# Kernel tuning notes

Measured on AMD Instinct MI355X. Metric: run time of the kernel, lower is better.

## Reference

```python
import jax, jax.numpy as jnp
import numpy as np

B, T, NMELS = 2, 2048, 64
D, H, DH, M, L = 256, 4, 64, 384, 4
FF2 = 2 * 4 * D  # GLU doubles the 4*dim hidden


def _layernorm(x, g, b):
    m = x.mean(-1, keepdims=True)
    v = ((x - m) ** 2).mean(-1, keepdims=True)
    return (x - m) * jax.lax.rsqrt(v + 1e-5) * g + b


def _conv(h, w, groups=1, pad='VALID'):
    return jax.lax.conv_general_dilated(h, w, (1, 1), pad, feature_group_count=groups,
                                        dimension_numbers=('NCHW', 'OIHW', 'NCHW'))


def _bn(h, g, b, m, v):
    return (h - m[:, None, None]) * jax.lax.rsqrt(v[:, None, None] + 1e-5) * g[:, None, None] + b[:, None, None]


def setup_inputs():
    key = jax.random.key(0)
    ks = jax.random.split(key, 40)
    def n(i, shape, s):
        return (jax.random.normal(ks[i], shape) * s).astype(jnp.float32)
    z = lambda shape: jnp.zeros(shape, jnp.float32)
    o = lambda shape: jnp.ones(shape, jnp.float32)
    return dict(
        x=n(0, (B, T, NMELS), 1.0),
        conv0_w=n(1, (4, 1, 1, 1), 0.5),
        dw1_w=n(2, (4, 1, 3, 3), 0.3), dw1_b=z(4),
        pw1_w=n(3, (D // 2, 4, 1, 1), 0.5), pw1_b=z(D // 2),
        bn1_g=o(D // 2), bn1_b=z(D // 2), bn1_m=n(4, (D // 2,), 0.05), bn1_v=o(D // 2),
        dw2_w=n(5, (D // 2, 1, 3, 3), 0.3), dw2_b=z(D // 2),
        pw2_w=n(6, (D, D // 2, 1, 1), 0.1), pw2_b=z(D),
        bn2_g=o(D), bn2_b=z(D), bn2_m=n(7, (D,), 0.05), bn2_v=o(D),
        proj_w=n(8, (D, D), 0.06), proj_b=z(D),
        ln0_g=o(D), ln0_b=z(D),
        pos_emb=n(9, (1, T, D), 0.02),
        ln1_g=o((L, D)), ln1_b=z((L, D)),
        wq=n(10, (L, D, D), 0.06), bq=z((L, D)),
        wk=n(11, (L, D, D), 0.06), bk=z((L, D)),
        wv=n(12, (L, D, D), 0.06), bv=z((L, D)),
        wo=n(13, (L, D, D), 0.06), bo=z((L, D)),
        proj_mat=n(14, (L, M, DH), 1.0),
        ln2_g=o((L, D)), ln2_b=z((L, D)),
        ffw1=n(15, (L, D, FF2), 0.06), ffb1=z((L, FF2)),
        ffw2=n(16, (L, FF2 // 2, D), 0.03), ffb2=z((L, D)),
        clf_w1=n(17, (D, D // 2), 0.06), clf_b1=z(D // 2),
        clf_ln_g=o(D // 2), clf_ln_b=z(D // 2),
        clf_w2=n(18, (D // 2, 1), 0.09), clf_b2=z(1),
    )


def reference(x, conv0_w, dw1_w, dw1_b, pw1_w, pw1_b, bn1_g, bn1_b, bn1_m, bn1_v,
              dw2_w, dw2_b, pw2_w, pw2_b, bn2_g, bn2_b, bn2_m, bn2_v,
              proj_w, proj_b, ln0_g, ln0_b, pos_emb,
              ln1_g, ln1_b, wq, bq, wk, bk, wv, bv, wo, bo, proj_mat,
              ln2_g, ln2_b, ffw1, ffb1, ffw2, ffb2,
              clf_w1, clf_b1, clf_ln_g, clf_ln_b, clf_w2, clf_b2):
    pad1 = ((1, 1), (1, 1))
    # conv frontend: [B,T,n_mels] -> [B,1,n_mels,T]
    h = x.transpose(0, 2, 1)[:, None]
    h = _conv(h, conv0_w)
    h = _conv(h, dw1_w, groups=4, pad=pad1) + dw1_b[:, None, None]
    h = _conv(h, pw1_w) + pw1_b[:, None, None]
    h = jax.nn.relu(_bn(h, bn1_g, bn1_b, bn1_m, bn1_v))
    h = _conv(h, dw2_w, groups=D // 2, pad=pad1) + dw2_b[:, None, None]
    h = _conv(h, pw2_w) + pw2_b[:, None, None]
    h = jax.nn.relu(_bn(h, bn2_g, bn2_b, bn2_m, bn2_v))
    h = h.mean(axis=2).transpose(0, 2, 1)  # [B,T,D]
    h = h @ proj_w + proj_b
    h = _layernorm(h, ln0_g, ln0_b) + pos_emb[:, :h.shape[1]]
    # reversible Performer: streams x1 (attn) / x2 (ff), combined by sum
    x1, x2 = h, h
    dn = DH ** -0.25
    for l in range(L):
        a = _layernorm(x2, ln1_g[l], ln1_b[l])
        Bsz, N, _ = a.shape
        q = (a @ wq[l] + bq[l]).reshape(Bsz, N, H, DH).transpose(0, 2, 1, 3)
        k = (a @ wk[l] + bk[l]).reshape(Bsz, N, H, DH).transpose(0, 2, 1, 3)
        v = (a @ wv[l] + bv[l]).reshape(Bsz, N, H, DH).transpose(0, 2, 1, 3)
        # FAVOR+ generalized (ReLU) kernel feature maps, eps=1e-3
        qf = jax.nn.relu(jnp.einsum('bhnd,jd->bhnj', dn * q, proj_mat[l])) + 1e-3
        kf = jax.nn.relu(jnp.einsum('bhnd,jd->bhnj', dn * k, proj_mat[l])) + 1e-3
        d_inv = 1.0 / jnp.einsum('bhnj,bhj->bhn', qf, kf.sum(axis=2))
        ctx = jnp.einsum('bhnj,bhnd->bhjd', kf, v)
        o = jnp.einsum('bhjd,bhnj,bhn->bhnd', ctx, qf, d_inv)
        o = o.transpose(0, 2, 1, 3).reshape(Bsz, N, D)
        x1 = x1 + (o @ wo[l] + bo[l])
        f = _layernorm(x1, ln2_g[l], ln2_b[l])
        u1, u2 = jnp.split(f @ ffw1[l] + ffb1[l], 2, axis=-1)
        x2 = x2 + (jax.nn.gelu(u1, approximate=False) * u2) @ ffw2[l] + ffb2[l]
    h = x1 + x2
    c = jax.nn.relu(_layernorm(h @ clf_w1 + clf_b1, clf_ln_g, clf_ln_b))
    return (c @ clf_w2 + clf_b2)[..., 0]
```

## Files before the change

### kernel.cpp

```cpp
#include <hip/hip_runtime.h>
#include <hip/hip_bf16.h>
#include <math.h>

using bf16 = __hip_bfloat16;
typedef __attribute__((ext_vector_type(8))) short short8;
typedef __attribute__((ext_vector_type(4))) float f32x4;

__device__ __forceinline__ float tof(float x) { return x; }
__device__ __forceinline__ float tof(bf16 x) { return __bfloat162float(x); }
__device__ __forceinline__ float b2f(unsigned short u) {
  union { float f; unsigned int i; } c; c.i = ((unsigned int)u) << 16; return c.f;
}
__device__ __forceinline__ unsigned short f2bu(float v) {
  bf16 h = __float2bfloat16(v);
  return *(unsigned short*)&h;
}
__device__ __forceinline__ void sto1(float* p, float v) { *p = v; }
__device__ __forceinline__ void sto1(bf16* p, float v) { *p = __float2bfloat16(v); }

__device__ __forceinline__ float gelu_exact(float x) {
  return 0.5f * x * (1.f + erff(x * 0.70710678118654752f));
}

__device__ __forceinline__ void llds16(const bf16* g, short* l) {
  __builtin_amdgcn_global_load_lds((const __attribute__((address_space(1))) void*)g,
                                   (__attribute__((address_space(3))) void*)l, 16, 0, 0);
}

__global__ __launch_bounds__(256) void pack_qkv_kernel(
    const float* __restrict__ wq, const float* __restrict__ wk,
    const float* __restrict__ wv, bf16* __restrict__ out)
{
  int idx = blockIdx.x * 256 + threadIdx.x;
  int k = idx & 255;
  int nl = idx >> 8;
  int n = nl % 768, l = nl / 768;
  const float* src = (n < 256) ? wq : (n < 512 ? wk : wv);
  out[idx] = __float2bfloat16(src[(long)l * 65536 + k * 256 + (n & 255)]);
}

__global__ __launch_bounds__(256) void pack_qkvbias_kernel(
    const float* __restrict__ bq, const float* __restrict__ bk,
    const float* __restrict__ bv, float* __restrict__ out)
{
  int i = blockIdx.x * 256 + threadIdx.x;
  if (i >= 3072) return;
  int n = i % 768, l = i / 768;
  const float* src = (n < 256) ? bq : (n < 512 ? bk : bv);
  out[i] = src[l * 256 + (n & 255)];
}

__global__ __launch_bounds__(256) void tconv_kernel(
    const float* __restrict__ in, bf16* __restrict__ out,
    int K, int N, long sin, long sout)
{
  int l = blockIdx.z;
  int idx = blockIdx.x * 256 + threadIdx.x;
  int k = idx % K, n = idx / K;
  out[l * sout + idx] = __float2bfloat16(in[l * sin + (long)k * N + n]);
}

__global__ __launch_bounds__(256) void f2b_kernel(
    const float* __restrict__ in, bf16* __restrict__ out, int n)
{
  int i = blockIdx.x * 256 + threadIdx.x;
  if (i < n) out[i] = __float2bfloat16(in[i]);
}

__global__ __launch_bounds__(256) void sumb_kernel(
    const float* __restrict__ a, const float* __restrict__ b, bf16* __restrict__ o)
{
  int i = (blockIdx.x * 256 + threadIdx.x) * 4;
  float4 x = *(const float4*)&a[i];
  float4 y = *(const float4*)&b[i];
  ushort4 p;
  p.x = f2bu(x.x + y.x); p.y = f2bu(x.y + y.y);
  p.z = f2bu(x.z + y.z); p.w = f2bu(x.w + y.w);
  *(ushort4*)((unsigned short*)o + i) = p;
}

__global__ __launch_bounds__(256) void front1_kernel(
    const float* __restrict__ x, const float* __restrict__ c0w,
    const float* __restrict__ d1w, const float* __restrict__ d1b,
    const float* __restrict__ p1w, const float* __restrict__ p1b,
    const float* __restrict__ g1, const float* __restrict__ b1,
    const float* __restrict__ m1, const float* __restrict__ v1,
    bf16* __restrict__ A1)
{
  __shared__ float sd[256];
  __shared__ float spw[512];
  __shared__ float ss[128], st[128], sb[128];
  int tid = threadIdx.x;
  int bt = blockIdx.x;
  int b = bt >> 11, t = bt & 2047;
  if (tid < 128) {
    float s = g1[tid] * rsqrtf(v1[tid] + 1e-5f);
    ss[tid] = s;
    st[tid] = b1[tid] - m1[tid] * s;
    sb[tid] = p1b[tid];
#pragma unroll
    for (int c = 0; c < 4; ++c) spw[c * 128 + tid] = p1w[tid * 4 + c];
  }
  {
    int c = tid >> 6, f = tid & 63;
    float cw = c0w[c];
    float acc = d1b[c];
#pragma unroll
    for (int kh = 0; kh < 3; ++kh) {
      int fi = f + kh - 1;
      if (fi < 0 || fi >= 64) continue;
#pragma unroll
      for (int kw = 0; kw < 3; ++kw) {
        int ti = t + kw - 1;
        if (ti < 0 || ti >= 2048) continue;
        acc += d1w[c * 9 + kh * 3 + kw] * cw * x[((long)b * 2048 + ti) * 64 + fi];
      }
    }
    sd[c * 64 + f] = acc;
  }
  __syncthreads();
  long ob = (long)bt * 8192;
  for (int it = 0; it < 32; ++it) {
    int o = it * 256 + tid;
    int f = o >> 7, ci = o & 127;
    float pre = sb[ci];
#pragma unroll
    for (int c = 0; c < 4; ++c) pre = fmaf(spw[c * 128 + ci], sd[c * 64 + f], pre);
    A1[ob + o] = __float2bfloat16(fmaxf(fmaf(ss[ci], pre, st[ci]), 0.f));
  }
}

__global__ __launch_bounds__(256) void convtail_kernel(
    const bf16* __restrict__ A1, const float* __restrict__ w,
    const float* __restrict__ wb, const bf16* __restrict__ w2b,
    const float* __restrict__ pb, const float* __restrict__ g2,
    const float* __restrict__ b2, const float* __restrict__ m2,
    const float* __restrict__ v2, bf16* __restrict__ hconvb)
{
  __shared__ short dw2s[64 * 136];
  __shared__ short Bs[64 * 136];
  __shared__ float red[16 * 64];
  __shared__ float swf[1152];
  __shared__ float sbias[128], ssc[64], ssh[64];
  int tid = threadIdx.x;
  int lane = tid & 63, wv = tid >> 6;
  int quad = lane >> 4, l15 = lane & 15;
  int rw = (wv >> 1) * 32, cw = (wv & 1) * 32;
  int bt = blockIdx.x, b = bt >> 11, t = bt & 2047;
  for (int l = tid; l < 1152; l += 256) swf[l] = w[(l & 127) * 9 + (l >> 7)];
  if (tid < 128) sbias[tid] = wb[tid];
  __syncthreads();
  const unsigned short* A1u = (const unsigned short*)A1;
  for (int pass = 0; pass < 8; ++pass) {
    int idx = pass * 256 + tid;
    int f = idx >> 5, ci4 = (idx & 31) * 4;
    float a0 = sbias[ci4], a1 = sbias[ci4 + 1], a2 = sbias[ci4 + 2], a3 = sbias[ci4 + 3];
#pragma unroll
    for (int kh = 0; kh < 3; ++kh) {
      int fi = f + kh - 1;
      if (fi < 0 || fi >= 64) continue;
#pragma unroll
      for (int kw = 0; kw < 3; ++kw) {
        int ti = t + kw - 1;
        if (ti < 0 || ti >= 2048) continue;
        ushort4 u = *(const ushort4*)&A1u[(((long)b * 2048 + ti) * 64 + fi) * 128 + ci4];
        int wi = (kh * 3 + kw) * 128 + ci4;
        a0 = fmaf(swf[wi],     b2f(u.x), a0);
        a1 = fmaf(swf[wi + 1], b2f(u.y), a1);
        a2 = fmaf(swf[wi + 2], b2f(u.z), a2);
        a3 = fmaf(swf[wi + 3], b2f(u.w), a3);
      }
    }
    ushort4 p; p.x = f2bu(a0); p.y = f2bu(a1); p.z = f2bu(a2); p.w = f2bu(a3);
    *(ushort4*)&dw2s[f * 136 + ci4] = p;
  }
  for (int ct = 0; ct < 4; ++ct) {
    int co0 = ct * 64;
    __syncthreads();
    for (int l2 = 0; l2 < 4; ++l2) {
      int idx = l2 * 256 + tid;
      int row = idx >> 4, koff = (idx & 15) * 8;
      *(short8*)&Bs[row * 136 + koff] =
          *(const short8*)&w2b[(long)(co0 + row) * 128 + koff];
    }
    if (tid < 64) {
      int co = co0 + tid;
      float s = g2[co] * rsqrtf(v2[co] + 1e-5f);
      ssc[tid] = s;
      ssh[tid] = b2[co] - m2[co] * s + s * pb[co];
    }
    __syncthreads();
    f32x4 zv = {0.f, 0.f, 0.f, 0.f};
    f32x4 acc[2][2] = {{zv, zv}, {zv, zv}};
#pragma unroll
    for (int kc = 0; kc < 4; ++kc) {
      short8 a0 = *(const short8*)&dw2s[(rw + l15) * 136 + kc * 32 + quad * 8];
      short8 a1 = *(const short8*)&dw2s[(rw + 16 + l15) * 136 + kc * 32 + quad * 8];
      short8 b0 = *(const short8*)&Bs[(cw + l15) * 136 + kc * 32 + quad * 8];
      short8 b1 = *(const short8*)&Bs[(cw + 16 + l15) * 136 + kc * 32 + quad * 8];
      acc[0][0] = __builtin_amdgcn_mfma_f32_16x16x32_bf16(a0, b0, acc[0][0], 0, 0, 0);
      acc[0][1] = __builtin_amdgcn_mfma_f32_16x16x32_bf16(a0, b1, acc[0][1], 0, 0, 0);
      acc[1][0] = __builtin_amdgcn_mfma_f32_16x16x32_bf16(a1, b0, acc[1][0], 0, 0, 0);
      acc[1][1] = __builtin_amdgcn_mfma_f32_16x16x32_bf16(a1, b1, acc[1][1], 0, 0, 0);
    }
#pragma unroll
    for (int mi = 0; mi < 2; ++mi)
#pragma unroll
      for (int nj = 0; nj < 2; ++nj) {
        int colg = cw + nj * 16 + l15;
        float s = ssc[colg], sh = ssh[colg];
        float sum = 0.f;
#pragma unroll
        for (int r = 0; r < 4; ++r) sum += fmaxf(fmaf(s, acc[mi][nj][r], sh), 0.f);
        int rowgroup = (wv >> 1) * 8 + mi * 4 + quad;
        red[rowgroup * 64 + colg] = sum;
      }
    __syncthreads();
    if (tid < 64) {
      float s = 0.f;
#pragma unroll
      for (int r = 0; r < 16; ++r) s += red[r * 64 + tid];
      hconvb[(long)bt * 256 + co0 + tid] = __float2bfloat16(s * (1.f / 64.f));
    }
  }
}

template <typename CTy, int EPI>
__global__ __launch_bounds__(256) void mgemm_kernel(
    const bf16* __restrict__ A, const bf16* __restrict__ Bt,
    const float* __restrict__ bias, const float* __restrict__ res,
    const float* __restrict__ rowsc, CTy* __restrict__ C, bf16* __restrict__ C2,
    int K, int lda, int ldbt, int ldc,
    long sAb, long sAh, long sBb, long sBh, long sCb, long sCh,
    long sRb, long sRh, int Hdiv, float alpha)
{
  __shared__ short As[4096];
  __shared__ short Bs[4096];
  int tid = threadIdx.x;
  int lane = tid & 63, w = tid >> 6;
  int quad = lane >> 4, l15 = lane & 15;
  int rw = (w >> 1) * 32, cw = (w & 1) * 32;
  int r0 = blockIdx.x * 64, n0 = blockIdx.y * 64;
  int zb = blockIdx.z / Hdiv, zh = blockIdx.z % Hdiv;
  A += zb * sAb + zh * sAh;
  Bt += zb * sBb + zh * sBh;
  C += zb * sCb + zh * sCh;
  if (res) res += zb * sCb + zh * sCh;
  const float* rsp = rowsc ? rowsc + zb * sRb + zh * sRh : nullptr;
  f32x4 zv = {0.f, 0.f, 0.f, 0.f};
  f32x4 acc[2][2] = {{zv, zv}, {zv, zv}};
  const bf16* Ag = A + (long)(r0 + (tid >> 2)) * lda + ((tid & 3) * 8);
  const bf16* Bg = Bt + (long)(n0 + (tid >> 2)) * ldbt + ((tid & 3) * 8);
  short* Asd = &As[tid * 8];
  short* Bsd = &Bs[tid * 8];
  for (int k0 = 0; k0 < K; k0 += 64) {
    if (k0) __syncthreads();
    llds16(Ag + k0, Asd);
    llds16(Ag + k0 + 32, Asd + 2048);
    llds16(Bg + k0, Bsd);
    llds16(Bg + k0 + 32, Bsd + 2048);
    __syncthreads();
#pragma unroll
    for (int c = 0; c < 2; ++c) {
      short8 a0 = *(const short8*)&As[c * 2048 + (rw + l15) * 32 + quad * 8];
      short8 a1 = *(const short8*)&As[c * 2048 + (rw + 16 + l15) * 32 + quad * 8];
      short8 b0 = *(const short8*)&Bs[c * 2048 + (cw + l15) * 32 + quad * 8];
      short8 b1 = *(const short8*)&Bs[c * 2048 + (cw + 16 + l15) * 32 + quad * 8];
      acc[0][0] = __builtin_amdgcn_mfma_f32_16x16x32_bf16(a0, b0, acc[0][0], 0, 0, 0);
      acc[0][1] = __builtin_amdgcn_mfma_f32_16x16x32_bf16(a0, b1, acc[0][1], 0, 0, 0);
      acc[1][0] = __builtin_amdgcn_mfma_f32_16x16x32_bf16(a1, b0, acc[1][0], 0, 0, 0);
      acc[1][1] = __builtin_amdgcn_mfma_f32_16x16x32_bf16(a1, b1, acc[1][1], 0, 0, 0);
    }
  }
#pragma unroll
  for (int mi = 0; mi < 2; ++mi)
#pragma unroll
    for (int nj = 0; nj < 2; ++nj) {
      int colg = n0 + cw + nj * 16 + l15;
      float bv_ = bias ? bias[colg] : 0.f;
      int rbase = r0 + rw + mi * 16 + quad * 4;
      float ov[4];
#pragma unroll
      for (int r = 0; r < 4; ++r) {
        float v = acc[mi][nj][r];
        if constexpr (EPI == 0 || EPI == 5) {
          v += bv_;
        } else if constexpr (EPI == 1) {
          v += bv_ + res[(long)(rbase + r) * ldc + colg];
        } else if constexpr (EPI == 2 || EPI == 6) {
          v = fmaxf(v * alpha, 0.f) + 1e-3f;
        } else if constexpr (EPI == 3) {
          v *= rsp[rbase + r];
        } else if constexpr (EPI == 4) {
          v = gelu_exact(v + bv_) * res[(long)(rbase + r) * ldc + colg];
        }
        ov[r] = v;
      }
      if constexpr (EPI == 6) {
        ushort4 p;
        p.x = f2bu(ov[0]); p.y = f2bu(ov[1]); p.z = f2bu(ov[2]); p.w = f2bu(ov[3]);
        *(ushort4*)((unsigned short*)C + (long)colg * ldc + rbase) = p;
      } else if constexpr (EPI == 5) {
        if (colg < 512) {
#pragma unroll
          for (int r = 0; r < 4; ++r) sto1(&C[(long)(rbase + r) * ldc + colg], ov[r]);
        } else {
          int bb = rbase >> 11, t0 = rbase & 2047;
          long off = (((long)bb * 4 + ((colg - 512) >> 6)) * 64 + (colg & 63)) * 2048 + t0;
          ushort4 p;
          p.x = f2bu(ov[0]); p.y = f2bu(ov[1]); p.z = f2bu(ov[2]); p.w = f2bu(ov[3]);
          *(ushort4*)((unsigned short*)C2 + off) = p;
        }
      } else {
#pragma unroll
        for (int r = 0; r < 4; ++r) sto1(&C[(long)(rbase + r) * ldc + colg], ov[r]);
      }
    }
  (void)alpha;
}

template <int DIM, bool RELU, bool ADDPOS, bool DUAL, typename OTy>
__global__ __launch_bounds__(256) void ln_kernel(
    const float* __restrict__ in, const float* __restrict__ g,
    const float* __restrict__ b, const float* __restrict__ pos,
    OTy* __restrict__ out0, float* __restrict__ out1)
{
  constexpr int CH = DIM / 64;
  int row = blockIdx.x * 4 + (threadIdx.x >> 6);
  int lane = threadIdx.x & 63;
  const float* rp = in + (long)row * DIM + lane * CH;
  float v[CH];
#pragma unroll
  for (int i = 0; i < CH; ++i) v[i] = rp[i];
  float s = 0.f;
#pragma unroll
  for (int i = 0; i < CH; ++i) s += v[i];
#pragma unroll
  for (int o = 32; o > 0; o >>= 1) s += __shfl_xor(s, o, 64);
  float mean = s * (1.f / DIM);
  float q = 0.f;
#pragma unroll
  for (int i = 0; i < CH; ++i) { float d = v[i] - mean; q += d * d; }
#pragma unroll
  for (int o = 32; o > 0; o >>= 1) q += __shfl_xor(q, o, 64);
  float rstd = rsqrtf(q * (1.f / DIM) + 1e-5f);
  int t = row & 2047;
#pragma unroll
  for (int i = 0; i < CH; ++i) {
    int c = lane * CH + i;
    float o = (v[i] - mean) * rstd * g[c] + b[c];
    if constexpr (ADDPOS) o += pos[(long)t * DIM + c];
    if constexpr (RELU) o = fmaxf(o, 0.f);
    sto1(&out0[(long)row * DIM + c], o);
    if constexpr (DUAL) out1[(long)row * DIM + c] = o;
  }
}

__global__ __launch_bounds__(256) void rowsum_kernel(
    const bf16* __restrict__ kfT, float* __restrict__ ksum)
{
  int z = blockIdx.x;
  int j = blockIdx.y * 4 + (threadIdx.x >> 6);
  int lane = threadIdx.x & 63;
  const short* base = (const short*)kfT + ((long)z * 384 + j) * 2048;
  float acc = 0.f;
#pragma unroll
  for (int i = 0; i < 4; ++i) {
    short8 v = *(const short8*)&base[i * 512 + lane * 8];
#pragma unroll
    for (int e = 0; e < 8; ++e) acc += b2f((unsigned short)v[e]);
  }
#pragma unroll
  for (int o = 32; o > 0; o >>= 1) acc += __shfl_xor(acc, o, 64);
  if (lane == 0) ksum[z * 384 + j] = acc;
}

__global__ __launch_bounds__(256) void dinv_kernel(
    const bf16* __restrict__ qf, const float* __restrict__ ksum,
    float* __restrict__ dinv)
{
  int z = blockIdx.x;
  int t = blockIdx.y * 4 + (threadIdx.x >> 6);
  int lane = threadIdx.x & 63;
  const bf16* qr = qf + ((long)z * 2048 + t) * 384;
  const float* ks = ksum + z * 384;
  float acc = 0.f;
#pragma unroll
  for (int i = 0; i < 6; ++i) {
    int j = lane + i * 64;
    acc = fmaf(tof(qr[j]), ks[j], acc);
  }
#pragma unroll
  for (int o = 32; o > 0; o >>= 1) acc += __shfl_xor(acc, o, 64);
  if (lane == 0) dinv[z * 2048 + t] = 1.f / acc;
}

__global__ __launch_bounds__(256) void clf2_kernel(
    const float* __restrict__ c2, const float* __restrict__ w,
    const float* __restrict__ b, float* __restrict__ out)
{
  int row = blockIdx.x * 4 + (threadIdx.x >> 6);
  int lane = threadIdx.x & 63;
  const float* rp = c2 + (long)row * 128 + lane * 2;
  float acc = rp[0] * w[lane * 2] + rp[1] * w[lane * 2 + 1];
#pragma unroll
  for (int o = 32; o > 0; o >>= 1) acc += __shfl_xor(acc, o, 64);
  if (lane == 0) out[row] = acc + b[0];
}

extern "C" void kernel_launch(void* const* d_in, const int* in_sizes, int n_in,
                              void* d_out, int out_size, void* d_ws, size_t ws_size,
                              hipStream_t stream)
{
  const float* X    = (const float*)d_in[0];
  const float* c0w  = (const float*)d_in[1];
  const float* d1w  = (const float*)d_in[2];
  const float* d1b  = (const float*)d_in[3];
  const float* p1w  = (const float*)d_in[4];
  const float* p1b  = (const float*)d_in[5];
  const float* g1   = (const float*)d_in[6];
  const float* b1   = (const float*)d_in[7];
  const float* m1   = (const float*)d_in[8];
  const float* v1   = (const float*)d_in[9];
  const float* d2w  = (const float*)d_in[10];
  const float* d2b  = (const float*)d_in[11];
  const float* p2w  = (const float*)d_in[12];
  const float* p2b  = (const float*)d_in[13];
  const float* g2   = (const float*)d_in[14];
  const float* b2   = (const float*)d_in[15];
  const float* m2   = (const float*)d_in[16];
  const float* v2   = (const float*)d_in[17];
  const float* projw= (const float*)d_in[18];
  const float* projb= (const float*)d_in[19];
  const float* ln0g = (const float*)d_in[20];
  const float* ln0b = (const float*)d_in[21];
  const float* pos  = (const float*)d_in[22];
  const float* ln1g = (const float*)d_in[23];
  const float* ln1b = (const float*)d_in[24];
  const float* wq   = (const float*)d_in[25];
  const float* bq   = (const float*)d_in[26];
  const float* wk   = (const float*)d_in[27];
  const float* bk   = (const float*)d_in[28];
  const float* wv   = (const float*)d_in[29];
  const float* bv   = (const float*)d_in[30];
  const float* wo   = (const float*)d_in[31];
  const float* bo   = (const float*)d_in[32];
  const float* pmat = (const float*)d_in[33];
  const float* ln2g = (const float*)d_in[34];
  const float* ln2b = (const float*)d_in[35];
  const float* ffw1 = (const float*)d_in[36];
  const float* ffb1 = (const float*)d_in[37];
  const float* ffw2 = (const float*)d_in[38];
  const float* ffb2 = (const float*)d_in[39];
  const float* cw1  = (const float*)d_in[40];
  const float* cb1  = (const float*)d_in[41];
  const float* clng = (const float*)d_in[42];
  const float* clnb = (const float*)d_in[43];
  const float* cw2  = (const float*)d_in[44];
  const float* cb2  = (const float*)d_in[45];
  (void)in_sizes; (void)n_in; (void)out_size; (void)ws_size;

  float* ws     = (float*)d_ws;
  float* x1     = ws;
  float* x2     = ws + 1048576;
  float* lnb32  = ws + 2097152;
  bf16*  lnb16  = (bf16*)(ws + 3145728);
  bf16*  hconvb = (bf16*)(ws + 3407872);
  bf16*  obufb  = (bf16*)(ws + 3670016);
  bf16*  qkvb   = (bf16*)(ws + 3932160);
  bf16*  vT     = (bf16*)(ws + 5505024);
  bf16*  qf     = (bf16*)(ws + 6029312);
  bf16*  kfT    = (bf16*)(ws + 9175040);
  bf16*  ctxT   = (bf16*)(ws + 12320768);
  float* ksum   = ws + 12419072;
  float* dinvp  = ws + 12423168;
  float* gbuf   = ws + 12439552;
  bf16*  gb2    = (bf16*)(ws + 16633856);
  bf16*  A1     = (bf16*)(ws + 3670016);
  bf16*  wqkv_bf= (bf16*)(ws + 20447232);
  float* qkvbias= ws + 20840448;
  bf16*  f1w_bf = (bf16*)(ws + 20843520);
  bf16*  f2w_bf = (bf16*)(ws + 21892096);
  bf16*  wo_bf  = (bf16*)(ws + 22416384);
  bf16*  pm_bf  = (bf16*)(ws + 22547456);
  bf16*  projwT = (bf16*)(ws + 22596608);
  bf16*  cw1T   = (bf16*)(ws + 22629376);
  bf16*  pw2_bf = (bf16*)(ws + 22645760);
  bf16*  sbuf   = qkvb;
  float* c1     = gbuf;
  float* c2     = gbuf + 524288;

  const float dn = 0.35355339059327378f;

  pack_qkv_kernel<<<3072, 256, 0, stream>>>(wq, wk, wv, wqkv_bf);
  pack_qkvbias_kernel<<<12, 256, 0, stream>>>(bq, bk, bv, qkvbias);
  tconv_kernel<<<dim3(2048, 1, 4), 256, 0, stream>>>(ffw1, f1w_bf, 256, 2048, 524288, 524288);
  tconv_kernel<<<dim3(1024, 1, 4), 256, 0, stream>>>(ffw2, f2w_bf, 1024, 256, 262144, 262144);
  tconv_kernel<<<dim3(256, 1, 4), 256, 0, stream>>>(wo, wo_bf, 256, 256, 65536, 65536);
  tconv_kernel<<<dim3(256, 1, 1), 256, 0, stream>>>(projw, projwT, 256, 256, 65536, 65536);
  tconv_kernel<<<dim3(128, 1, 1), 256, 0, stream>>>(cw1, cw1T, 256, 128, 32768, 32768);
  f2b_kernel<<<384, 256, 0, stream>>>(pmat, pm_bf, 98304);
  f2b_kernel<<<128, 256, 0, stream>>>(p2w, pw2_bf, 32768);

  front1_kernel<<<4096, 256, 0, stream>>>(X, c0w, d1w, d1b, p1w, p1b, g1, b1, m1, v1, A1);
  convtail_kernel<<<4096, 256, 0, stream>>>(A1, d2w, d2b, pw2_bf, p2b, g2, b2, m2, v2, hconvb);

  mgemm_kernel<float, 0><<<dim3(64, 4, 1), 256, 0, stream>>>(
      hconvb, projwT, projb, nullptr, nullptr, lnb32, nullptr,
      256, 256, 256, 256, 0, 0, 0, 0, 0, 0, 0, 0, 1, 1.f);
  ln_kernel<256, false, true, true, float><<<1024, 256, 0, stream>>>(
      lnb32, ln0g, ln0b, pos, x1, x2);

  for (int l = 0; l < 4; ++l) {
    const bf16* wqkv_l = wqkv_bf + (size_t)l * 196608;
    const float* qb_l  = qkvbias + l * 768;
    const bf16* pm_l   = pm_bf + (size_t)l * 24576;
    const bf16* wo_l   = wo_bf + (size_t)l * 65536;
    const float* bov   = bo + l * 256;
    const bf16* f1w_l  = f1w_bf + (size_t)l * 524288;
    const float* f1b_l = ffb1 + l * 2048;
    const bf16* f2w_l  = f2w_bf + (size_t)l * 262144;
    const float* f2b_l = ffb2 + l * 256;

    ln_kernel<256, false, false, false, bf16><<<1024, 256, 0, stream>>>(
        x2, ln1g + l * 256, ln1b + l * 256, nullptr, lnb16, nullptr);
    mgemm_kernel<bf16, 5><<<dim3(64, 12, 1), 256, 0, stream>>>(
        lnb16, wqkv_l, qb_l, nullptr, nullptr, qkvb, vT,
        256, 256, 256, 768, 0, 0, 0, 0, 0, 0, 0, 0, 1, 1.f);
    mgemm_kernel<bf16, 2><<<dim3(32, 6, 8), 256, 0, stream>>>(
        qkvb, pm_l, nullptr, nullptr, nullptr, qf, nullptr,
        64, 768, 64, 384, 1572864, 64, 0, 0, 3145728, 786432, 0, 0, 4, dn);
    mgemm_kernel<bf16, 6><<<dim3(32, 6, 8), 256, 0, stream>>>(
        qkvb + 256, pm_l, nullptr, nullptr, nullptr, kfT, nullptr,
        64, 768, 64, 2048, 1572864, 64, 0, 0, 6291456, 1572864, 0, 0, 4, dn);
    rowsum_kernel<<<dim3(8, 96), 256, 0, stream>>>(kfT, ksum);
    dinv_kernel<<<dim3(8, 512), 256, 0, stream>>>(qf, ksum, dinvp);
    mgemm_kernel<bf16, 0><<<dim3(1, 6, 8), 256, 0, stream>>>(
        vT, kfT, nullptr, nullptr, nullptr, ctxT, nullptr,
        2048, 2048, 2048, 384, 524288, 131072, 3145728, 786432, 98304, 24576, 0, 0, 4, 1.f);
    mgemm_kernel<bf16, 3><<<dim3(32, 1, 8), 256, 0, stream>>>(
        qf, ctxT, nullptr, nullptr, dinvp, obufb, nullptr,
        384, 384, 384, 256, 3145728, 786432, 98304, 24576, 524288, 64, 8192, 2048, 4, 1.f);
    mgemm_kernel<float, 1><<<dim3(64, 4, 1), 256, 0, stream>>>(
        obufb, wo_l, bov, x1, nullptr, x1, nullptr,
        256, 256, 256, 256, 0, 0, 0, 0, 0, 0, 0, 0, 1, 1.f);
    ln_kernel<256, false, false, false, bf16><<<1024, 256, 0, stream>>>(
        x1, ln2g + l * 256, ln2b + l * 256, nullptr, lnb16, nullptr);
    mgemm_kernel<float, 0><<<dim3(64, 16, 1), 256, 0, stream>>>(
        lnb16, f1w_l + 1024 * 256, f1b_l + 1024, nullptr, nullptr, gbuf, nullptr,
        256, 256, 256, 1024, 0, 0, 0, 0, 0, 0, 0, 0, 1, 1.f);
    mgemm_kernel<bf16, 4><<<dim3(64, 16, 1), 256, 0, stream>>>(
        lnb16, f1w_l, f1b_l, gbuf, nullptr, gb2, nullptr,
        256, 256, 256, 1024, 0, 0, 0, 0, 0, 0, 0, 0, 1, 1.f);
    mgemm_kernel<float, 1><<<dim3(64, 4, 1), 256, 0, stream>>>(
        gb2, f2w_l, f2b_l, x2, nullptr, x2, nullptr,
        1024, 1024, 1024, 256, 0, 0, 0, 0, 0, 0, 0, 0, 1, 1.f);
  }

  sumb_kernel<<<1024, 256, 0, stream>>>(x1, x2, sbuf);
  mgemm_kernel<float, 0><<<dim3(64, 2, 1), 256, 0, stream>>>(
      sbuf, cw1T, cb1, nullptr, nullptr, c1, nullptr,
      256, 256, 256, 128, 0, 0, 0, 0, 0, 0, 0, 0, 1, 1.f);
  ln_kernel<128, true, false, false, float><<<1024, 256, 0, stream>>>(
      c1, clng, clnb, nullptr, c2, nullptr);
  clf2_kernel<<<1024, 256, 0, stream>>>(c2, cw2, cb2, (float*)d_out);
}
```

Baseline: 779.7 us.

## Split-K ctx GEMM with atomics, fuse GLU halves into one GEMM, register conv weights

The ctx GEMM (K=2048, only 48 blocks) becomes a split-K launch of 384 blocks that accumulate into an fp32 buffer with atomicAdd. This needs an added zeroing kernel and an fp32-to-bf16 conversion pass. The two GLU FFN-up GEMMs are fused into one kernel that loads both weight halves and applies gelu(u1)*u2 in the epilogue, which removes the fp32 gbuf round-trip. The convtail depthwise weights and bias move from shared memory into registers, dropping a sync.

```diff
diff --git a/kernel.cpp b/kernel.cpp
--- a/kernel.cpp
+++ b/kernel.cpp
@@ -65,6 +65,12 @@
 {
   int i = blockIdx.x * 256 + threadIdx.x;
   if (i < n) out[i] = __float2bfloat16(in[i]);
+}
+
+__global__ __launch_bounds__(256) void zero4_kernel(float* __restrict__ p) {
+  int i = (blockIdx.x * 256 + threadIdx.x) * 4;
+  float4 z; z.x = 0.f; z.y = 0.f; z.z = 0.f; z.w = 0.f;
+  *(float4*)&p[i] = z;
 }
 
 __global__ __launch_bounds__(256) void sumb_kernel(
@@ -139,22 +145,25 @@
 {
   __shared__ short dw2s[64 * 136];
   __shared__ short Bs[64 * 136];
-  __shared__ float red[16 * 64];
-  __shared__ float swf[1152];
-  __shared__ float sbias[128], ssc[64], ssh[64];
+  __shared__ float red[1024];
+  __shared__ float ssc[64], ssh[64];
   int tid = threadIdx.x;
   int lane = tid & 63, wv = tid >> 6;
   int quad = lane >> 4, l15 = lane & 15;
   int rw = (wv >> 1) * 32, cw = (wv & 1) * 32;
   int bt = blockIdx.x, b = bt >> 11, t = bt & 2047;
-  for (int l = tid; l < 1152; l += 256) swf[l] = w[(l & 127) * 9 + (l >> 7)];
-  if (tid < 128) sbias[tid] = wb[tid];
-  __syncthreads();
+  int ci4 = (tid & 31) * 4;
+  float wreg[9][4], breg[4];
+#pragma unroll
+  for (int c = 0; c < 4; ++c) {
+    breg[c] = wb[ci4 + c];
+#pragma unroll
+    for (int kk = 0; kk < 9; ++kk) wreg[kk][c] = w[(ci4 + c) * 9 + kk];
+  }
   const unsigned short* A1u = (const unsigned short*)A1;
   for (int pass = 0; pass < 8; ++pass) {
-    int idx = pass * 256 + tid;
-    int f = idx >> 5, ci4 = (idx & 31) * 4;
-    float a0 = sbias[ci4], a1 = sbias[ci4 + 1], a2 = sbias[ci4 + 2], a3 = sbias[ci4 + 3];
+    int f = pass * 8 + (tid >> 5);
+    float a0 = breg[0], a1 = breg[1], a2 = breg[2], a3 = breg[3];
 #pragma unroll
     for (int kh = 0; kh < 3; ++kh) {
       int fi = f + kh - 1;
@@ -164,11 +173,11 @@
         int ti = t + kw - 1;
         if (ti < 0 || ti >= 2048) continue;
         ushort4 u = *(const ushort4*)&A1u[(((long)b * 2048 + ti) * 64 + fi) * 128 + ci4];
-        int wi = (kh * 3 + kw) * 128 + ci4;
-        a0 = fmaf(swf[wi],     b2f(u.x), a0);
-        a1 = fmaf(swf[wi + 1], b2f(u.y), a1);
-        a2 = fmaf(swf[wi + 2], b2f(u.z), a2);
-        a3 = fmaf(swf[wi + 3], b2f(u.w), a3);
+        int kk = kh * 3 + kw;
+        a0 = fmaf(wreg[kk][0], b2f(u.x), a0);
+        a1 = fmaf(wreg[kk][1], b2f(u.y), a1);
+        a2 = fmaf(wreg[kk][2], b2f(u.z), a2);
+        a3 = fmaf(wreg[kk][3], b2f(u.w), a3);
       }
     }
     ushort4 p; p.x = f2bu(a0); p.y = f2bu(a1); p.z = f2bu(a2); p.w = f2bu(a3);
@@ -236,6 +245,7 @@
 {
   __shared__ short As[4096];
   __shared__ short Bs[4096];
+  __shared__ short Bs2[(EPI == 8) ? 4096 : 8];
   int tid = threadIdx.x;
   int lane = tid & 63, w = tid >> 6;
   int quad = lane >> 4, l15 = lane & 15;
@@ -246,19 +256,26 @@
   Bt += zb * sBb + zh * sBh;
   C += zb * sCb + zh * sCh;
   if (res) res += zb * sCb + zh * sCh;
-  const float* rsp = rowsc ? rowsc + zb * sRb + zh * sRh : nullptr;
+  const float* rsp = (EPI == 3) ? rowsc + zb * sRb + zh * sRh : nullptr;
   f32x4 zv = {0.f, 0.f, 0.f, 0.f};
   f32x4 acc[2][2] = {{zv, zv}, {zv, zv}};
+  f32x4 acc2[2][2] = {{zv, zv}, {zv, zv}};
   const bf16* Ag = A + (long)(r0 + (tid >> 2)) * lda + ((tid & 3) * 8);
   const bf16* Bg = Bt + (long)(n0 + (tid >> 2)) * ldbt + ((tid & 3) * 8);
+  const bf16* Bg2 = (EPI == 8) ? Bg + sRb : nullptr;
   short* Asd = &As[tid * 8];
   short* Bsd = &Bs[tid * 8];
+  short* Bs2d = &Bs2[(EPI == 8) ? tid * 8 : 0];
   for (int k0 = 0; k0 < K; k0 += 64) {
     if (k0) __syncthreads();
     llds16(Ag + k0, Asd);
     llds16(Ag + k0 + 32, Asd + 2048);
     llds16(Bg + k0, Bsd);
     llds16(Bg + k0 + 32, Bsd + 2048);
+    if constexpr (EPI == 8) {
+      llds16(Bg2 + k0, Bs2d);
+      llds16(Bg2 + k0 + 32, Bs2d + 2048);
+    }
     __syncthreads();
 #pragma unroll
     for (int c = 0; c < 2; ++c) {
@@ -270,6 +287,14 @@
       acc[0][1] = __builtin_amdgcn_mfma_f32_16x16x32_bf16(a0, b1, acc[0][1], 0, 0, 0);
       acc[1][0] = __builtin_amdgcn_mfma_f32_16x16x32_bf16(a1, b0, acc[1][0], 0, 0, 0);
       acc[1][1] = __builtin_amdgcn_mfma_f32_16x16x32_bf16(a1, b1, acc[1][1], 0, 0, 0);
+      if constexpr (EPI == 8) {
+        short8 c0 = *(const short8*)&Bs2[c * 2048 + (cw + l15) * 32 + quad * 8];
+        short8 c1 = *(const short8*)&Bs2[c * 2048 + (cw + 16 + l15) * 32 + quad * 8];
+        acc2[0][0] = __builtin_amdgcn_mfma_f32_16x16x32_bf16(a0, c0, acc2[0][0], 0, 0, 0);
+        acc2[0][1] = __builtin_amdgcn_mfma_f32_16x16x32_bf16(a0, c1, acc2[0][1], 0, 0, 0);
+        acc2[1][0] = __builtin_amdgcn_mfma_f32_16x16x32_bf16(a1, c0, acc2[1][0], 0, 0, 0);
+        acc2[1][1] = __builtin_amdgcn_mfma_f32_16x16x32_bf16(a1, c1, acc2[1][1], 0, 0, 0);
+      }
     }
   }
 #pragma unroll
@@ -278,6 +303,7 @@
     for (int nj = 0; nj < 2; ++nj) {
       int colg = n0 + cw + nj * 16 + l15;
       float bv_ = bias ? bias[colg] : 0.f;
+      float bv2 = (EPI == 8) ? bias[colg + 1024] : 0.f;
       int rbase = r0 + rw + mi * 16 + quad * 4;
       float ov[4];
 #pragma unroll
@@ -293,6 +319,8 @@
           v *= rsp[rbase + r];
         } else if constexpr (EPI == 4) {
           v = gelu_exact(v + bv_) * res[(long)(rbase + r) * ldc + colg];
+        } else if constexpr (EPI == 8) {
+          v = gelu_exact(v + bv_) * (acc2[mi][nj][r] + bv2);
         }
         ov[r] = v;
       }
@@ -311,6 +339,10 @@
           p.x = f2bu(ov[0]); p.y = f2bu(ov[1]); p.z = f2bu(ov[2]); p.w = f2bu(ov[3]);
           *(ushort4*)((unsigned short*)C2 + off) = p;
         }
+      } else if constexpr (EPI == 7) {
+#pragma unroll
+        for (int r = 0; r < 4; ++r)
+          atomicAdd((float*)&C[(long)(rbase + r) * ldc + colg], ov[r]);
       } else {
 #pragma unroll
         for (int r = 0; r < 4; ++r) sto1(&C[(long)(rbase + r) * ldc + colg], ov[r]);
@@ -471,10 +503,12 @@
   bf16*  vT     = (bf16*)(ws + 5505024);
   bf16*  qf     = (bf16*)(ws + 6029312);
   bf16*  kfT    = (bf16*)(ws + 9175040);
-  bf16*  ctxT   = (bf16*)(ws + 12320768);
-  float* ksum   = ws + 12419072;
-  float* dinvp  = ws + 12423168;
-  float* gbuf   = ws + 12439552;
+  float* ctx32  = ws + 12320768;
+  float* ksum   = ws + 12517376;
+  float* dinvp  = ws + 12521472;
+  bf16*  ctxb   = (bf16*)(ws + 12537856);
+  float* c1     = ws + 12587008;
+  float* c2     = ws + 13111296;
   bf16*  gb2    = (bf16*)(ws + 16633856);
   bf16*  A1     = (bf16*)(ws + 3670016);
   bf16*  wqkv_bf= (bf16*)(ws + 20447232);
@@ -487,8 +521,6 @@
   bf16*  cw1T   = (bf16*)(ws + 22629376);
   bf16*  pw2_bf = (bf16*)(ws + 22645760);
   bf16*  sbuf   = qkvb;
-  float* c1     = gbuf;
-  float* c2     = gbuf + 524288;
 
   const float dn = 0.35355339059327378f;
 
@@ -535,23 +567,22 @@
         64, 768, 64, 2048, 1572864, 64, 0, 0, 6291456, 1572864, 0, 0, 4, dn);
     rowsum_kernel<<<dim3(8, 96), 256, 0, stream>>>(kfT, ksum);
     dinv_kernel<<<dim3(8, 512), 256, 0, stream>>>(qf, ksum, dinvp);
-    mgemm_kernel<bf16, 0><<<dim3(1, 6, 8), 256, 0, stream>>>(
-        vT, kfT, nullptr, nullptr, nullptr, ctxT, nullptr,
-        2048, 2048, 2048, 384, 524288, 131072, 3145728, 786432, 98304, 24576, 0, 0, 4, 1.f);
+    zero4_kernel<<<192, 256, 0, stream>>>(ctx32);
+    mgemm_kernel<float, 7><<<dim3(1, 6, 64), 256, 0, stream>>>(
+        vT, kfT, nullptr, nullptr, nullptr, ctx32, nullptr,
+        256, 2048, 2048, 384, 131072, 256, 786432, 256, 24576, 0, 0, 0, 8, 1.f);
+    f2b_kernel<<<768, 256, 0, stream>>>(ctx32, ctxb, 196608);
     mgemm_kernel<bf16, 3><<<dim3(32, 1, 8), 256, 0, stream>>>(
-        qf, ctxT, nullptr, nullptr, dinvp, obufb, nullptr,
+        qf, ctxb, nullptr, nullptr, dinvp, obufb, nullptr,
         384, 384, 384, 256, 3145728, 786432, 98304, 24576, 524288, 64, 8192, 2048, 4, 1.f);
     mgemm_kernel<float, 1><<<dim3(64, 4, 1), 256, 0, stream>>>(
         obufb, wo_l, bov, x1, nullptr, x1, nullptr,
         256, 256, 256, 256, 0, 0, 0, 0, 0, 0, 0, 0, 1, 1.f);
     ln_kernel<256, false, false, false, bf16><<<1024, 256, 0, stream>>>(
         x1, ln2g + l * 256, ln2b + l * 256, nullptr, lnb16, nullptr);
-    mgemm_kernel<float, 0><<<dim3(64, 16, 1), 256, 0, stream>>>(
-        lnb16, f1w_l + 1024 * 256, f1b_l + 1024, nullptr, nullptr, gbuf, nullptr,
-        256, 256, 256, 1024, 0, 0, 0, 0, 0, 0, 0, 0, 1, 1.f);
-    mgemm_kernel<bf16, 4><<<dim3(64, 16, 1), 256, 0, stream>>>(
-        lnb16, f1w_l, f1b_l, gbuf, nullptr, gb2, nullptr,
-        256, 256, 256, 1024, 0, 0, 0, 0, 0, 0, 0, 0, 1, 1.f);
+    mgemm_kernel<bf16, 8><<<dim3(64, 16, 1), 256, 0, stream>>>(
+        lnb16, f1w_l, f1b_l, nullptr, nullptr, gb2, nullptr,
+        256, 256, 256, 1024, 0, 0, 0, 0, 0, 0, 262144, 0, 1, 1.f);
     mgemm_kernel<float, 1><<<dim3(64, 4, 1), 256, 0, stream>>>(
         gb2, f2w_l, f2b_l, x2, nullptr, x2, nullptr,
         1024, 1024, 1024, 256, 0, 0, 0, 0, 0, 0, 0, 0, 1, 1.f);
```

After: 680.9 us. 12.7% less time.
